# Optimization experiments

Hardware: AMD Instinct MI355X
Metric: run time of the kernel (lower is better)

Reference implementation:

```python
import jax, jax.numpy as jnp
import numpy as np
import math

HIDDEN = 2048
HIGHWAY_BIAS = 0.0
# rescale=True, has_skip_term=True, num_matrices=3 -> residual scaled by sqrt(1+2*exp(bias))
SCALE_X = (1.0 + 2.0 * math.exp(HIGHWAY_BIAS)) ** 0.5


def setup_inputs() -> dict:
    key = jax.random.key(0)
    k1, k2, k3 = jax.random.split(key, 3)
    L, B, D = 1024, 8, HIDDEN
    x = jax.random.normal(k1, (L, B, D), dtype=jnp.float32)
    c0 = jnp.zeros((B, D), dtype=jnp.float32)
    # Xavier-like init scale as in reset_parameters (uniform +-sqrt(3/D))
    val_range = (3.0 / D) ** 0.5
    weight = jax.random.uniform(k2, (D, 3 * D), dtype=jnp.float32,
                                minval=-val_range, maxval=val_range)
    weight_c = jax.random.uniform(k3, (2 * D,), dtype=jnp.float32,
                                  minval=-(3.0 ** 0.5), maxval=3.0 ** 0.5) * (0.5 ** 0.5)
    bias = jnp.concatenate([jnp.zeros((D,), jnp.float32),
                            jnp.full((D,), HIGHWAY_BIAS, jnp.float32)])
    return {"x": x, "c0": c0, "weight": weight, "weight_c": weight_c, "bias": bias}


def _sru_forward(x, c0, weight, weight_c, bias):
    L, B, D = x.shape
    # U = x @ W  -> [L, B, 3, D]; num_matrices=3 (input_size == output_size)
    U = jnp.einsum('lbi,ij->lbj', x, weight).reshape(L, B, D, 3)
    u0 = U[..., 0]  # candidate
    u1 = U[..., 1]  # forget gate pre-activation
    u2 = U[..., 2]  # reset/highway gate pre-activation
    vf, vr = weight_c[:D], weight_c[D:]
    bf, br = bias[:D], bias[D:]

    def step(c_prev, inp):
        u0t, u1t, u2t, xt = inp
        f = jax.nn.sigmoid(u1t + vf * c_prev + bf)
        c_t = (c_prev - u0t) * f + u0t
        r = jax.nn.sigmoid(u2t + vr * c_t + br)
        # activation 'none': g(c_t) = c_t; skip term = x * scale_x
        h_t = r * c_t + (1.0 - r) * xt * SCALE_X
        return c_t, h_t

    c_last, h = jax.lax.scan(step, c0, (u0, u1, u2, x))
    return h, c_last


def reference(x, c0, weight, weight_c, bias):
    return _sru_forward(x, c0, weight, weight_c, bias)
```

## Files before the change

kernel.cpp:

```cpp
#include <hip/hip_runtime.h>
#include <stdint.h>

#define L_SEQ 1024
#define BATCH 8
#define DIM   2048
#define GM    8192
#define GN    6144
#define GK    2048
#define SCALE_X 1.7320508075688772f
#define SCAN_PF 16
#define W_ILV  8192

using bf16x8  = __attribute__((ext_vector_type(8))) __bf16;
using floatx4 = __attribute__((ext_vector_type(4))) float;

__device__ __forceinline__ unsigned short f2bf(float f) {
  unsigned u = __float_as_uint(f);
  u += 0x7FFFu + ((u >> 16) & 1u);
  return (unsigned short)(u >> 16);
}
__device__ __forceinline__ float sigmoidf_fast(float z) {
  return __builtin_amdgcn_rcpf(1.0f + __expf(-z));
}
__device__ __forceinline__ void async16(const unsigned short* g, unsigned short* l) {
  __builtin_amdgcn_global_load_lds(
      (__attribute__((address_space(1))) unsigned int*)g,
      (__attribute__((address_space(3))) unsigned int*)l,
      16, 0, 0);
}

template <bool ILV>
__global__ __launch_bounds__(256) void cast_x_kernel(const float4* __restrict__ xin,
                                                     unsigned short* __restrict__ Aout,
                                                     unsigned short* __restrict__ Ux) {
  const int n4 = (GM * GK) / 4;
  for (int i = blockIdx.x * blockDim.x + threadIdx.x; i < n4; i += gridDim.x * blockDim.x) {
    float4 v = xin[i];
    union { unsigned short s[4]; unsigned long long ll; } o;
    o.s[0] = f2bf(v.x); o.s[1] = f2bf(v.y); o.s[2] = f2bf(v.z); o.s[3] = f2bf(v.w);
    *(unsigned long long*)&Aout[(size_t)i * 4] = o.ll;
    if (ILV) {
      const int f = i * 4;
      const int gm = f >> 11, d = f & (DIM - 1);
      unsigned short* dst = Ux + (size_t)gm * W_ILV + 2 * d + 1;
      dst[0] = o.s[0]; dst[2] = o.s[1]; dst[4] = o.s[2]; dst[6] = o.s[3];
    }
  }
}

__global__ __launch_bounds__(256) void transpose_w_kernel(const float* __restrict__ W,
                                                          unsigned short* __restrict__ Bt) {
  __shared__ float tile[32][33];
  const int tx = threadIdx.x & 31, ty = threadIdx.x >> 5;
  const int n0 = blockIdx.x * 32;
  const int k0 = blockIdx.y * 32;
#pragma unroll
  for (int r = 0; r < 32; r += 8)
    tile[ty + r][tx] = W[(size_t)(k0 + ty + r) * GN + n0 + tx];
  __syncthreads();
#pragma unroll
  for (int r = 0; r < 32; r += 8) {
    const int n = n0 + ty + r;
    const int dq = n / 3, j = n - 3 * dq;
    const int np = (j == 0) ? dq : (DIM + 2 * dq + (j - 1));
    Bt[(size_t)np * GK + k0 + tx] = f2bf(tile[tx][ty + r]);
  }
}

template <bool ILV>
__global__ __launch_bounds__(256) void gemm_kernel(const unsigned short* __restrict__ A,
                                                   const unsigned short* __restrict__ Bt,
                                                   unsigned short* __restrict__ U) {
  __shared__ alignas(16) unsigned short As[128 * 64];
  __shared__ alignas(16) unsigned short Bs[128 * 64];
  const int tid  = threadIdx.x;
  const int wave = tid >> 6, lane = tid & 63;
  const int quad = lane >> 4, lrow = lane & 15;
  const int wm = (wave >> 1) * 64, wn = (wave & 1) * 64;
  const int mBase = blockIdx.y * 128, nBase = blockIdx.x * 128;

  floatx4 acc[4][4] = {};

  const int r  = tid >> 3;
  const int sC = tid & 7;
  const int cg = sC ^ (r & 7);
  const unsigned short* aG0 = A  + (size_t)(mBase + r) * GK + cg * 8;
  const unsigned short* bG0 = Bt + (size_t)(nBase + r) * GK + cg * 8;
  unsigned short* asD = &As[tid * 8];
  unsigned short* bsD = &Bs[tid * 8];
  const int swz = lrow & 7;

  for (int k0 = 0; k0 < GK; k0 += 64) {
#pragma unroll
    for (int i = 0; i < 4; ++i) async16(aG0 + (size_t)i * 32 * GK + k0, asD + i * 2048);
#pragma unroll
    for (int i = 0; i < 4; ++i) async16(bG0 + (size_t)i * 32 * GK + k0, bsD + i * 2048);
    __syncthreads();

#pragma unroll
    for (int kk = 0; kk < 2; ++kk) {
      const int s = (kk * 4 + quad) ^ swz;
      bf16x8 aF[4], bF[4];
#pragma unroll
      for (int t = 0; t < 4; ++t) {
        aF[t] = *(const bf16x8*)&As[(wm + t * 16 + lrow) * 64 + s * 8];
        bF[t] = *(const bf16x8*)&Bs[(wn + t * 16 + lrow) * 64 + s * 8];
      }
#pragma unroll
      for (int mt = 0; mt < 4; ++mt)
#pragma unroll
        for (int nt = 0; nt < 4; ++nt)
          acc[mt][nt] = __builtin_amdgcn_mfma_f32_16x16x32_bf16(aF[mt], bF[nt], acc[mt][nt], 0, 0, 0);
    }
    __syncthreads();
  }

  const int rowW = ILV ? W_ILV : GN;
#pragma unroll
  for (int mt = 0; mt < 4; ++mt) {
    const int gm = mBase + wm + mt * 16 + quad * 4;
#pragma unroll
    for (int nt = 0; nt < 4; ++nt) {
      const int gn = nBase + wn + nt * 16 + lrow;
      const int col = ILV ? ((gn < DIM) ? 2 * gn : gn + DIM) : gn;
#pragma unroll
      for (int q = 0; q < 4; ++q)
        U[(size_t)(gm + q) * rowW + col] = f2bf(acc[mt][nt][q]);
    }
  }
}

__global__ __launch_bounds__(64) void sru_scan_ilv(const unsigned short* __restrict__ U,
                                                   const float* __restrict__ c0,
                                                   const float* __restrict__ wc,
                                                   const float* __restrict__ bias,
                                                   float* __restrict__ out) {
  const int e = blockIdx.x * 64 + threadIdx.x;
  const int b = e >> 11, d = e & (DIM - 1);
  const float vf = wc[d], vr = wc[DIM + d];
  const float bfv = bias[d], brv = bias[DIM + d];
  float c = c0[e];

  constexpr int PF = SCAN_PF;
  constexpr int UD = BATCH * W_ILV / 2;
  constexpr int XS = BATCH * DIM;

  const unsigned* u0x = (const unsigned*)(U + (size_t)b * W_ILV + 2 * d);
  const unsigned* u12 = (const unsigned*)(U + (size_t)b * W_ILV + 2 * DIM + 2 * d);
  float* hp = out + (size_t)b * DIM + d;

  unsigned p0x[PF], p12[PF];
#pragma unroll
  for (int j = 0; j < PF; ++j) {
    p0x[j] = u0x[(size_t)j * UD];
    p12[j] = u12[(size_t)j * UD];
  }
  const unsigned* f0x = u0x + (size_t)PF * UD;
  const unsigned* f12 = u12 + (size_t)PF * UD;

  for (int l0 = 0; l0 < L_SEQ; l0 += PF) {
#pragma unroll
    for (int j = 0; j < PF; ++j) {
      const unsigned ra = p0x[j], rb = p12[j];
      p0x[j] = *f0x; p12[j] = *f12;
      f0x += UD; f12 += UD;
      const float a0 = __uint_as_float(ra << 16);
      const float ax = __uint_as_float(ra & 0xFFFF0000u) * SCALE_X;
      const float u1 = __uint_as_float(rb << 16);
      const float u2 = __uint_as_float(rb & 0xFFFF0000u);
      const float f = sigmoidf_fast(u1 + fmaf(vf, c, bfv));
      c = fmaf(c - a0, f, a0);
      const float rr = sigmoidf_fast(u2 + fmaf(vr, c, brv));
      *hp = fmaf(rr, c - ax, ax);
      hp += XS;
    }
  }
  out[(size_t)L_SEQ * XS + e] = c;
}

__global__ __launch_bounds__(64) void sru_scan_flat(const unsigned short* __restrict__ U,
                                                    const unsigned short* __restrict__ xbf,
                                                    const float* __restrict__ c0,
                                                    const float* __restrict__ wc,
                                                    const float* __restrict__ bias,
                                                    float* __restrict__ out) {
  const int e = blockIdx.x * 64 + threadIdx.x;
  const int b = e >> 11, d = e & (DIM - 1);
  const float vf = wc[d], vr = wc[DIM + d];
  const float bfv = bias[d], brv = bias[DIM + d];
  float c = c0[e];

  constexpr int PF = SCAN_PF;
  constexpr int US = BATCH * GN;
  constexpr int XS = BATCH * DIM;

  const unsigned short* u0p  = U + (size_t)b * GN + d;
  const unsigned short* u12p = U + (size_t)b * GN + DIM + 2 * d;
  const unsigned short* xp   = xbf + (size_t)b * DIM + d;
  float* hp = out + (size_t)b * DIM + d;

  unsigned pu0[PF], pu12[PF], pux[PF];
#pragma unroll
  for (int j = 0; j < PF; ++j) {
    pu0[j]  = u0p[(size_t)j * US];
    pu12[j] = *(const unsigned*)(u12p + (size_t)j * US);
    pux[j]  = xp[(size_t)j * XS];
  }
  const unsigned short* uf0  = u0p + (size_t)PF * US;
  const unsigned short* uf12 = u12p + (size_t)PF * US;
  const unsigned short* xf   = xp + (size_t)PF * XS;

  for (int l0 = 0; l0 < L_SEQ; l0 += PF) {
#pragma unroll
    for (int j = 0; j < PF; ++j) {
      const unsigned r0 = pu0[j], r12 = pu12[j], rx = pux[j];
      pu0[j]  = uf0[0];
      pu12[j] = *(const unsigned*)uf12;
      pux[j]  = xf[0];
      uf0 += US; uf12 += US; xf += XS;
      const float a0 = __uint_as_float(r0 << 16);
      const float u1 = __uint_as_float(r12 << 16);
      const float u2 = __uint_as_float(r12 & 0xFFFF0000u);
      const float ax = __uint_as_float(rx << 16) * SCALE_X;
      const float f = sigmoidf_fast(u1 + fmaf(vf, c, bfv));
      c = fmaf(c - a0, f, a0);
      const float rr = sigmoidf_fast(u2 + fmaf(vr, c, brv));
      *hp = fmaf(rr, c - ax, ax);
      hp += XS;
    }
  }
  out[(size_t)L_SEQ * XS + e] = c;
}

extern "C" void kernel_launch(void* const* d_in, const int* in_sizes, int n_in,
                              void* d_out, int out_size, void* d_ws, size_t ws_size,
                              hipStream_t stream) {
  const float* x    = (const float*)d_in[0];
  const float* c0   = (const float*)d_in[1];
  const float* W    = (const float*)d_in[2];
  const float* wc   = (const float*)d_in[3];
  const float* bias = (const float*)d_in[4];
  float* out = (float*)d_out;

  char* ws = (char*)d_ws;
  const size_t ILV_NEED = 33554432u + 25165824u + 134217728u + 2097152u;

  if (ws_size >= ILV_NEED) {
    unsigned short* A_bf  = (unsigned short*)(ws);
    unsigned short* Bt_bf = (unsigned short*)(ws + 33554432);
    unsigned short* U_bf  = (unsigned short*)(ws + 58720256);
    cast_x_kernel<true><<<4096, 256, 0, stream>>>((const float4*)x, A_bf, U_bf);
    transpose_w_kernel<<<dim3(GN / 32, GK / 32), 256, 0, stream>>>(W, Bt_bf);
    gemm_kernel<true><<<dim3(GN / 128, GM / 128), 256, 0, stream>>>(A_bf, Bt_bf, U_bf);
    sru_scan_ilv<<<256, 64, 0, stream>>>(U_bf, c0, wc, bias, out);
  } else {
    unsigned short* A_bf  = (unsigned short*)(ws);
    unsigned short* Bt_bf = (unsigned short*)(ws + 34078720);
    unsigned short* U_bf  = (unsigned short*)(ws + 59244544);
    cast_x_kernel<false><<<4096, 256, 0, stream>>>((const float4*)x, A_bf, nullptr);
    transpose_w_kernel<<<dim3(GN / 32, GK / 32), 256, 0, stream>>>(W, Bt_bf);
    gemm_kernel<false><<<dim3(GN / 128, GM / 128), 256, 0, stream>>>(A_bf, Bt_bf, U_bf);
    sru_scan_flat<<<256, 64, 0, stream>>>(U_bf, A_bf, c0, wc, bias, out);
  }
}
```

Measured before the change: 478.0 us.

## Store GEMM output time-contiguous per chain so the scan reads vectorized rows

The GEMM epilogue now writes U0 (packed with bf16 x) and the U1/U2 pair into layouts where each (batch, dim) chain's 1024 timesteps sit contiguously. The scan kernel can then stream them with 16-byte vector loads, double-buffered over 16-step chunks, instead of issuing one strided 4-byte load per step. The interleaved x write moves out of the cast kernel and into the GEMM epilogue. The cost is a scattered, uncoalesced epilogue: consecutive lanes write addresses 4 KB apart, plus an extra x gather, which could slow the GEMM.

```diff
diff --git a/kernel.cpp b/kernel.cpp
--- a/kernel.cpp
+++ b/kernel.cpp
@@ -8,8 +8,6 @@
 #define GN    6144
 #define GK    2048
 #define SCALE_X 1.7320508075688772f
-#define SCAN_PF 16
-#define W_ILV  8192
 
 using bf16x8  = __attribute__((ext_vector_type(8))) __bf16;
 using floatx4 = __attribute__((ext_vector_type(4))) float;
@@ -29,22 +27,14 @@
       16, 0, 0);
 }
 
-template <bool ILV>
 __global__ __launch_bounds__(256) void cast_x_kernel(const float4* __restrict__ xin,
-                                                     unsigned short* __restrict__ Aout,
-                                                     unsigned short* __restrict__ Ux) {
+                                                     unsigned short* __restrict__ Aout) {
   const int n4 = (GM * GK) / 4;
   for (int i = blockIdx.x * blockDim.x + threadIdx.x; i < n4; i += gridDim.x * blockDim.x) {
     float4 v = xin[i];
     union { unsigned short s[4]; unsigned long long ll; } o;
     o.s[0] = f2bf(v.x); o.s[1] = f2bf(v.y); o.s[2] = f2bf(v.z); o.s[3] = f2bf(v.w);
     *(unsigned long long*)&Aout[(size_t)i * 4] = o.ll;
-    if (ILV) {
-      const int f = i * 4;
-      const int gm = f >> 11, d = f & (DIM - 1);
-      unsigned short* dst = Ux + (size_t)gm * W_ILV + 2 * d + 1;
-      dst[0] = o.s[0]; dst[2] = o.s[1]; dst[4] = o.s[2]; dst[6] = o.s[3];
-    }
   }
 }
 
@@ -67,10 +57,13 @@
   }
 }
 
-template <bool ILV>
+template <bool TRN>
 __global__ __launch_bounds__(256) void gemm_kernel(const unsigned short* __restrict__ A,
                                                    const unsigned short* __restrict__ Bt,
-                                                   unsigned short* __restrict__ U) {
+                                                   unsigned short* __restrict__ U,
+                                                   unsigned* __restrict__ U0X,
+                                                   unsigned short* __restrict__ U12s,
+                                                   const unsigned short* __restrict__ Xbf) {
   __shared__ alignas(16) unsigned short As[128 * 64];
   __shared__ alignas(16) unsigned short Bs[128 * 64];
   const int tid  = threadIdx.x;
@@ -115,22 +108,47 @@
     __syncthreads();
   }
 
-  const int rowW = ILV ? W_ILV : GN;
-#pragma unroll
-  for (int mt = 0; mt < 4; ++mt) {
-    const int gm = mBase + wm + mt * 16 + quad * 4;
-#pragma unroll
-    for (int nt = 0; nt < 4; ++nt) {
-      const int gn = nBase + wn + nt * 16 + lrow;
-      const int col = ILV ? ((gn < DIM) ? 2 * gn : gn + DIM) : gn;
-#pragma unroll
-      for (int q = 0; q < 4; ++q)
-        U[(size_t)(gm + q) * rowW + col] = f2bf(acc[mt][nt][q]);
-    }
-  }
-}
-
-__global__ __launch_bounds__(64) void sru_scan_ilv(const unsigned short* __restrict__ U,
+  if (TRN) {
+    const bool isU0 = (nBase < DIM);
+#pragma unroll
+    for (int mt = 0; mt < 4; ++mt) {
+      const int gmB = mBase + wm + mt * 16 + quad * 4;
+#pragma unroll
+      for (int nt = 0; nt < 4; ++nt) {
+        const int gn = nBase + wn + nt * 16 + lrow;
+#pragma unroll
+        for (int q = 0; q < 4; ++q) {
+          const int gm = gmB + q;
+          const int l = gm >> 3, bb = gm & 7;
+          if (isU0) {
+            const int chain = bb * DIM + gn;
+            const unsigned xs = Xbf[(size_t)gm * GK + gn];
+            U0X[(size_t)chain * L_SEQ + l] = (unsigned)f2bf(acc[mt][nt][q]) | (xs << 16);
+          } else {
+            const int g2 = gn - DIM, dd = g2 >> 1, half = g2 & 1;
+            const int chain = bb * DIM + dd;
+            U12s[((size_t)chain * L_SEQ + l) * 2 + half] = f2bf(acc[mt][nt][q]);
+          }
+        }
+      }
+    }
+  } else {
+#pragma unroll
+    for (int mt = 0; mt < 4; ++mt) {
+      const int gm = mBase + wm + mt * 16 + quad * 4;
+#pragma unroll
+      for (int nt = 0; nt < 4; ++nt) {
+        const int gn = nBase + wn + nt * 16 + lrow;
+#pragma unroll
+        for (int q = 0; q < 4; ++q)
+          U[(size_t)(gm + q) * GN + gn] = f2bf(acc[mt][nt][q]);
+      }
+    }
+  }
+}
+
+__global__ __launch_bounds__(64) void sru_scan_trn(const unsigned* __restrict__ U0X,
+                                                   const unsigned* __restrict__ U12,
                                                    const float* __restrict__ c0,
                                                    const float* __restrict__ wc,
                                                    const float* __restrict__ bias,
@@ -140,39 +158,57 @@
   const float vf = wc[d], vr = wc[DIM + d];
   const float bfv = bias[d], brv = bias[DIM + d];
   float c = c0[e];
-
-  constexpr int PF = SCAN_PF;
-  constexpr int UD = BATCH * W_ILV / 2;
   constexpr int XS = BATCH * DIM;
-
-  const unsigned* u0x = (const unsigned*)(U + (size_t)b * W_ILV + 2 * d);
-  const unsigned* u12 = (const unsigned*)(U + (size_t)b * W_ILV + 2 * DIM + 2 * d);
   float* hp = out + (size_t)b * DIM + d;
 
-  unsigned p0x[PF], p12[PF];
-#pragma unroll
-  for (int j = 0; j < PF; ++j) {
-    p0x[j] = u0x[(size_t)j * UD];
-    p12[j] = u12[(size_t)j * UD];
-  }
-  const unsigned* f0x = u0x + (size_t)PF * UD;
-  const unsigned* f12 = u12 + (size_t)PF * UD;
-
-  for (int l0 = 0; l0 < L_SEQ; l0 += PF) {
-#pragma unroll
-    for (int j = 0; j < PF; ++j) {
-      const unsigned ra = p0x[j], rb = p12[j];
-      p0x[j] = *f0x; p12[j] = *f12;
-      f0x += UD; f12 += UD;
-      const float a0 = __uint_as_float(ra << 16);
-      const float ax = __uint_as_float(ra & 0xFFFF0000u) * SCALE_X;
-      const float u1 = __uint_as_float(rb << 16);
-      const float u2 = __uint_as_float(rb & 0xFFFF0000u);
-      const float f = sigmoidf_fast(u1 + fmaf(vf, c, bfv));
-      c = fmaf(c - a0, f, a0);
-      const float rr = sigmoidf_fast(u2 + fmaf(vr, c, brv));
-      *hp = fmaf(rr, c - ax, ax);
-      hp += XS;
+  const uint4* p0 = (const uint4*)(U0X + (size_t)e * L_SEQ);
+  const uint4* p1 = (const uint4*)(U12 + (size_t)e * L_SEQ);
+
+  uint4 X0[4], X1[4], Y0[4], Y1[4];
+#pragma unroll
+  for (int i = 0; i < 4; ++i) { X0[i] = p0[i];     X1[i] = p1[i]; }
+#pragma unroll
+  for (int i = 0; i < 4; ++i) { Y0[i] = p0[4 + i]; Y1[i] = p1[4 + i]; }
+
+#pragma unroll 1
+  for (int cb = 0; cb < 32; ++cb) {
+    const int nx = (2 * cb + 2) & 63;
+    const int ny = (2 * cb + 3) & 63;
+#pragma unroll
+    for (int i = 0; i < 4; ++i) {
+      const uint4 a = X0[i], u = X1[i];
+      X0[i] = p0[nx * 4 + i]; X1[i] = p1[nx * 4 + i];
+#pragma unroll
+      for (int j = 0; j < 4; ++j) {
+        const unsigned ra = (&a.x)[j], rb = (&u.x)[j];
+        const float a0 = __uint_as_float(ra << 16);
+        const float ax = __uint_as_float(ra & 0xFFFF0000u) * SCALE_X;
+        const float u1 = __uint_as_float(rb << 16);
+        const float u2 = __uint_as_float(rb & 0xFFFF0000u);
+        const float f = sigmoidf_fast(u1 + fmaf(vf, c, bfv));
+        c = fmaf(c - a0, f, a0);
+        const float rr = sigmoidf_fast(u2 + fmaf(vr, c, brv));
+        *hp = fmaf(rr, c - ax, ax);
+        hp += XS;
+      }
+    }
+#pragma unroll
+    for (int i = 0; i < 4; ++i) {
+      const uint4 a = Y0[i], u = Y1[i];
+      Y0[i] = p0[ny * 4 + i]; Y1[i] = p1[ny * 4 + i];
+#pragma unroll
+      for (int j = 0; j < 4; ++j) {
+        const unsigned ra = (&a.x)[j], rb = (&u.x)[j];
+        const float a0 = __uint_as_float(ra << 16);
+        const float ax = __uint_as_float(ra & 0xFFFF0000u) * SCALE_X;
+        const float u1 = __uint_as_float(rb << 16);
+        const float u2 = __uint_as_float(rb & 0xFFFF0000u);
+        const float f = sigmoidf_fast(u1 + fmaf(vf, c, bfv));
+        c = fmaf(c - a0, f, a0);
+        const float rr = sigmoidf_fast(u2 + fmaf(vr, c, brv));
+        *hp = fmaf(rr, c - ax, ax);
+        hp += XS;
+      }
     }
   }
   out[(size_t)L_SEQ * XS + e] = c;
@@ -190,7 +226,7 @@
   const float bfv = bias[d], brv = bias[DIM + d];
   float c = c0[e];
 
-  constexpr int PF = SCAN_PF;
+  constexpr int PF = 16;
   constexpr int US = BATCH * GN;
   constexpr int XS = BATCH * DIM;
 
@@ -243,23 +279,26 @@
   float* out = (float*)d_out;
 
   char* ws = (char*)d_ws;
-  const size_t ILV_NEED = 33554432u + 25165824u + 134217728u + 2097152u;
-
-  if (ws_size >= ILV_NEED) {
+  const size_t TRN_NEED = 33554432u + 25165824u + 67108864u + 67108864u;
+
+  if (ws_size >= TRN_NEED) {
     unsigned short* A_bf  = (unsigned short*)(ws);
     unsigned short* Bt_bf = (unsigned short*)(ws + 33554432);
-    unsigned short* U_bf  = (unsigned short*)(ws + 58720256);
-    cast_x_kernel<true><<<4096, 256, 0, stream>>>((const float4*)x, A_bf, U_bf);
+    unsigned*       U0X   = (unsigned*)(ws + 58720256);
+    unsigned*       U12   = (unsigned*)(ws + 125829120);
+    cast_x_kernel<<<4096, 256, 0, stream>>>((const float4*)x, A_bf);
     transpose_w_kernel<<<dim3(GN / 32, GK / 32), 256, 0, stream>>>(W, Bt_bf);
-    gemm_kernel<true><<<dim3(GN / 128, GM / 128), 256, 0, stream>>>(A_bf, Bt_bf, U_bf);
-    sru_scan_ilv<<<256, 64, 0, stream>>>(U_bf, c0, wc, bias, out);
+    gemm_kernel<true><<<dim3(GN / 128, GM / 128), 256, 0, stream>>>(
+        A_bf, Bt_bf, nullptr, U0X, (unsigned short*)U12, A_bf);
+    sru_scan_trn<<<256, 64, 0, stream>>>(U0X, U12, c0, wc, bias, out);
   } else {
     unsigned short* A_bf  = (unsigned short*)(ws);
     unsigned short* Bt_bf = (unsigned short*)(ws + 34078720);
     unsigned short* U_bf  = (unsigned short*)(ws + 59244544);
-    cast_x_kernel<false><<<4096, 256, 0, stream>>>((const float4*)x, A_bf, nullptr);
+    cast_x_kernel<<<4096, 256, 0, stream>>>((const float4*)x, A_bf);
     transpose_w_kernel<<<dim3(GN / 32, GK / 32), 256, 0, stream>>>(W, Bt_bf);
-    gemm_kernel<false><<<dim3(GN / 128, GM / 128), 256, 0, stream>>>(A_bf, Bt_bf, U_bf);
+    gemm_kernel<false><<<dim3(GN / 128, GM / 128), 256, 0, stream>>>(
+        A_bf, Bt_bf, U_bf, nullptr, nullptr, nullptr);
     sru_scan_flat<<<256, 64, 0, stream>>>(U_bf, A_bf, c0, wc, bias, out);
   }
 }
```

Result: slower. 590.3 us (+23.5%).
